# Performance work log

Hardware: AMD Instinct MI355X
Metric: run time of the kernel (lower is better)

Reference implementation:

```python
import jax, jax.numpy as jnp
import numpy as np
import math

D_MODEL = 1024
NUM_HEAD = 16
D_HEAD = D_MODEL // NUM_HEAD
SEQ = 2048
BATCH = 2


def setup_inputs() -> dict:
    key = jax.random.key(0)
    k1, k2, k3, k4, k5 = jax.random.split(key, 5)
    s = 1.0 / math.sqrt(D_MODEL)
    return {
        "x": jax.random.normal(k1, (SEQ, BATCH, D_MODEL), dtype=jnp.float32),
        "qkv_w": jax.random.normal(k2, (3 * D_MODEL, D_MODEL), dtype=jnp.float32) * s,
        "qkv_b": jax.random.normal(k3, (3 * D_MODEL,), dtype=jnp.float32) * 0.01,
        "out_w": jax.random.normal(k4, (D_MODEL, D_MODEL), dtype=jnp.float32) * s,
        "out_b": jax.random.normal(k5, (D_MODEL,), dtype=jnp.float32) * 0.01,
        "is_causal": 1,
    }


def reference(x, qkv_w, qkv_b, out_w, out_b, is_causal):
    t, b, _ = x.shape
    qkv = x @ qkv_w.T + qkv_b  # [t, b, 3*d_model]
    # 't b (k h d) -> b k h t d'
    qkv = qkv.reshape(t, b, 3, NUM_HEAD, D_HEAD).transpose(1, 2, 3, 0, 4)
    q, k, v = qkv[:, 0], qkv[:, 1], qkv[:, 2]  # each [b, h, t, d]
    softmax_scale = 1.0 / math.sqrt(D_HEAD)
    # NOTE: faithful to source bug: score is DIVIDED by softmax_scale
    score = jnp.einsum('bhtd,bhsd->bhts', q, k) / softmax_scale
    if is_causal:
        causal_mask = jnp.triu(jnp.full((t, t), -1000000.0, dtype=score.dtype), k=1)
        score = score + causal_mask
    attn = jax.nn.softmax(score, axis=-1)
    av = jnp.einsum('bhts,bhsd->bhtd', attn, v)  # [b, h, t, d]
    av = av.transpose(2, 0, 1, 3).reshape(t, b, D_MODEL)  # 'b h t d -> t b (h d)'
    return av @ out_w.T + out_b
```

## Files before the change

kernel.cpp:

```cpp
#include <hip/hip_runtime.h>
#include <math.h>

#define TSEQ   2048
#define BB     2
#define DMODEL 1024
#define NHEAD  16
#define DHEAD  64
#define MROWS  (TSEQ * BB)
#define NQB    (TSEQ / 64)

typedef __attribute__((ext_vector_type(8))) _Float16 half8;
typedef __attribute__((ext_vector_type(4))) float    floatx4;
typedef unsigned short u16;
typedef unsigned int   u32;

#define QSCL 11.5415603f
#define MSK  1442695.0f

__device__ __forceinline__ u16 f2h(float f) {
    union { _Float16 h; u16 u; } cv;
    cv.h = (_Float16)f;
    return cv.u;
}

__device__ __forceinline__ u32 pkrtz(float a, float b) {
    typedef __attribute__((ext_vector_type(2))) __fp16 fp16x2;
    union { fp16x2 h; u32 u; } cv;
    cv.h = __builtin_amdgcn_cvt_pkrtz(a, b);
    return cv.u;
}

__device__ __forceinline__ void async_cp16(const u16* g, u16* l) {
    __builtin_amdgcn_global_load_lds(
        (const __attribute__((address_space(1))) unsigned int*)g,
        (__attribute__((address_space(3))) unsigned int*)l, 16, 0, 0);
}

__global__ __launch_bounds__(256)
void cast3_f32_f16(const float* __restrict__ a, u16* __restrict__ oa,
                   const float* __restrict__ b, u16* __restrict__ ob,
                   const float* __restrict__ c, u16* __restrict__ oc)
{
    int i = blockIdx.x * 256 + threadIdx.x;
    const float* src; u16* dst; int off;
    if (i < 1048576)      { src = a; dst = oa; off = 0; }
    else if (i < 1835008) { src = b; dst = ob; off = 1048576; }
    else                  { src = c; dst = oc; off = 1835008; }
    int j = i - off;
    float4 v = ((const float4*)src)[j];
    ushort4 o;
    o.x = f2h(v.x); o.y = f2h(v.y); o.z = f2h(v.z); o.w = f2h(v.w);
    ((ushort4*)dst)[j] = o;
}

__global__ __launch_bounds__(256)
void gemm_qkv(const u16* __restrict__ A, const u16* __restrict__ W,
              const float* __restrict__ bias,
              u16* __restrict__ Qo, u16* __restrict__ Ko, u16* __restrict__ Vo,
              int M, int N, int K)
{
    __shared__ __align__(16) u16 As[128][64];
    __shared__ __align__(16) u16 Bs[64][64];

    const int tid  = threadIdx.x;
    const int lane = tid & 63;
    const int wv   = tid >> 6;
    const int ln   = lane & 15, lh = lane >> 4;
    const int m0   = blockIdx.y * 128;
    const int n0   = blockIdx.x * 64;

    const int c = n0 >> 10;
    const bool vmode = (c == 2);

    const int srowA = wv * 32 + (lane >> 3);
    const int srowW = wv * 16 + (lane >> 3);
    const int sslot = lane & 7;

    const floatx4 zero4 = {0.0f, 0.0f, 0.0f, 0.0f};
    floatx4 acc[2][4];
#pragma unroll
    for (int i = 0; i < 2; ++i)
#pragma unroll
        for (int j = 0; j < 4; ++j) acc[i][j] = zero4;

    for (int k0 = 0; k0 < K; k0 += 64) {
        __syncthreads();
#pragma unroll
        for (int t = 0; t < 4; ++t) {
            const int row = srowA + t * 8;
            const int g   = sslot ^ (row & 7);
            async_cp16(A + (size_t)(m0 + row) * K + k0 + g * 8, &As[row][sslot * 8]);
        }
#pragma unroll
        for (int t = 0; t < 2; ++t) {
            const int row = srowW + t * 8;
            const int g   = sslot ^ (row & 7);
            async_cp16(W + (size_t)(n0 + row) * K + k0 + g * 8, &Bs[row][sslot * 8]);
        }
        __syncthreads();

#pragma unroll
        for (int ks = 0; ks < 2; ++ks) {
            half8 xf[2], wf[4];
#pragma unroll
            for (int i = 0; i < 2; ++i) {
                const int row = wv * 32 + i * 16 + ln;
                xf[i] = *(const half8*)&As[row][(((ks << 2) | lh) ^ (row & 7)) * 8];
            }
#pragma unroll
            for (int j = 0; j < 4; ++j) {
                const int row = j * 16 + ln;
                wf[j] = *(const half8*)&Bs[row][(((ks << 2) | lh) ^ (row & 7)) * 8];
            }
            if (vmode) {
#pragma unroll
                for (int i = 0; i < 2; ++i)
#pragma unroll
                    for (int j = 0; j < 4; ++j)
                        acc[i][j] = __builtin_amdgcn_mfma_f32_16x16x32_f16(xf[i], wf[j], acc[i][j], 0, 0, 0);
            } else {
#pragma unroll
                for (int i = 0; i < 2; ++i)
#pragma unroll
                    for (int j = 0; j < 4; ++j)
                        acc[i][j] = __builtin_amdgcn_mfma_f32_16x16x32_f16(wf[j], xf[i], acc[i][j], 0, 0, 0);
            }
        }
    }

    if (!vmode) {
        const float scl = (c == 0) ? QSCL : 1.0f;
        u16* dst = (c == 0) ? Qo : Ko;
#pragma unroll
        for (int j = 0; j < 4; ++j) {
            const int nb = n0 + j * 16 + lh * 4;
            const float4 b4 = *(const float4*)&bias[nb];
            const int h  = (nb >> 6) & 15;
            const int d0 = nb & 63;
#pragma unroll
            for (int i = 0; i < 2; ++i) {
                const int tok = m0 + wv * 32 + i * 16 + ln;
                const int t = tok >> 1, b = tok & 1;
                uint2 pk;
                pk.x = pkrtz((acc[i][j][0] + b4.x) * scl, (acc[i][j][1] + b4.y) * scl);
                pk.y = pkrtz((acc[i][j][2] + b4.z) * scl, (acc[i][j][3] + b4.w) * scl);
                *(uint2*)&dst[(((size_t)b * NHEAD + h) * TSEQ + t) * DHEAD + d0] = pk;
            }
        }
    } else {
#pragma unroll
        for (int j = 0; j < 4; ++j) {
            const int col = n0 + j * 16 + ln;
            const float bc = bias[col];
            const int h = (col >> 6) & 15;
            const int d = col & 63;
#pragma unroll
            for (int i = 0; i < 2; ++i) {
                const int mb = m0 + wv * 32 + i * 16 + lh * 4;
                const int t0 = mb >> 1;
                const u32 e0 = pkrtz(acc[i][j][0] + bc, acc[i][j][2] + bc);
                const u32 e1 = pkrtz(acc[i][j][1] + bc, acc[i][j][3] + bc);
                *(u32*)&Vo[(((size_t)0 * NHEAD + h) * DHEAD + d) * TSEQ + t0] = e0;
                *(u32*)&Vo[(((size_t)1 * NHEAD + h) * DHEAD + d) * TSEQ + t0] = e1;
            }
        }
    }
}

__global__ __launch_bounds__(256)
void gemm_out64(const u16* __restrict__ A, const u16* __restrict__ W,
                const float* __restrict__ bias, float* __restrict__ Cout,
                int M, int N, int K)
{
    __shared__ __align__(16) u16 As[64][64];
    __shared__ __align__(16) u16 Bs[64][64];

    const int tid  = threadIdx.x;
    const int lane = tid & 63;
    const int wv   = tid >> 6;
    const int ln   = lane & 15, lh = lane >> 4;
    const int m0   = blockIdx.y * 64;
    const int n0   = blockIdx.x * 64;

    const floatx4 zero4 = {0.0f, 0.0f, 0.0f, 0.0f};
    floatx4 acc[4];
#pragma unroll
    for (int j = 0; j < 4; ++j) acc[j] = zero4;

    for (int k0 = 0; k0 < K; k0 += 64) {
        __syncthreads();
#pragma unroll
        for (int cb = 0; cb < 2; ++cb) {
            const int idx  = cb * 256 + tid;
            const int row  = idx >> 3;
            const int slot = idx & 7;
            const int g    = slot ^ (row & 7);
            async_cp16(A + (size_t)(m0 + row) * K + k0 + g * 8, &As[row][slot * 8]);
            async_cp16(W + (size_t)(n0 + row) * K + k0 + g * 8, &Bs[row][slot * 8]);
        }
        __syncthreads();

#pragma unroll
        for (int ks = 0; ks < 2; ++ks) {
            const int arow = wv * 16 + ln;
            half8 xf = *(const half8*)&As[arow][(((ks << 2) | lh) ^ (arow & 7)) * 8];
#pragma unroll
            for (int j = 0; j < 4; ++j) {
                const int row = j * 16 + ln;
                half8 wf = *(const half8*)&Bs[row][(((ks << 2) | lh) ^ (row & 7)) * 8];
                acc[j] = __builtin_amdgcn_mfma_f32_16x16x32_f16(wf, xf, acc[j], 0, 0, 0);
            }
        }
    }

#pragma unroll
    for (int j = 0; j < 4; ++j) {
        const int fb = n0 + j * 16 + lh * 4;
        const float4 b4 = *(const float4*)&bias[fb];
        const int tok = m0 + wv * 16 + ln;
        float4 v;
        v.x = acc[j][0] + b4.x;
        v.y = acc[j][1] + b4.y;
        v.z = acc[j][2] + b4.z;
        v.w = acc[j][3] + b4.w;
        *(float4*)&Cout[(size_t)tok * N + fb] = v;
    }
}

__global__ __launch_bounds__(256)
void flash_f16(const u16* __restrict__ Q, const u16* __restrict__ K,
               const u16* __restrict__ Vt, u16* __restrict__ AV,
               const int* __restrict__ causal_p)
{
    __shared__ __align__(16) u16 smem[(64 + 64 + 80) * 72];
    u16 (* __restrict__ QPs)[72] = (u16(*)[72])smem;
    u16 (* __restrict__ Ks)[72]  = (u16(*)[72])(smem + 64 * 72);
    u16 (* __restrict__ Vs)[72]  = (u16(*)[72])(smem + 128 * 72);

    const int tid  = threadIdx.x;
    const int lane = tid & 63;
    const int wv   = tid >> 6;
    const int ln   = lane & 15, lh = lane >> 4;

    const int phase = blockIdx.x >> 8;
    const int slot  = blockIdx.x & 255;
    const int bh    = slot & 31;
    const int jq    = slot >> 5;
    int qb;
    if      (phase == 0) qb = 31 - jq;
    else if (phase == 1) qb = jq;
    else if (phase == 2) qb = 23 - jq;
    else                 qb = 8 + jq;

    const int b = bh >> 4;
    const int h = bh & 15;
    const int causal = causal_p[0];

    const u16* Qg = Q  + (size_t)bh * TSEQ * DHEAD;
    const u16* Kg = K  + (size_t)bh * TSEQ * DHEAD;
    const u16* Vg = Vt + (size_t)bh * DHEAD * TSEQ;

    const int lrow = tid >> 3;
    const int lc8  = (tid & 7) * 8;

    *(uint4*)&QPs[lrow][lc8]      = *(const uint4*)(Qg + (size_t)(qb * 64 + lrow) * DHEAD + lc8);
    *(uint4*)&QPs[lrow + 32][lc8] = *(const uint4*)(Qg + (size_t)(qb * 64 + lrow + 32) * DHEAD + lc8);
    for (int idx = tid; idx < 16 * 72; idx += 256) {
        const int rr = idx / 72, cc = idx % 72;
        Vs[64 + rr][cc] = (rr == 0) ? (u16)0x3C00 : (u16)0;
    }
    uint4 kreg0 = *(const uint4*)(Kg + (size_t)lrow * DHEAD + lc8);
    uint4 kreg1 = *(const uint4*)(Kg + (size_t)(lrow + 32) * DHEAD + lc8);
    uint4 vreg0 = *(const uint4*)(Vg + (size_t)lrow * TSEQ + lc8);
    uint4 vreg1 = *(const uint4*)(Vg + (size_t)(lrow + 32) * TSEQ + lc8);
    __syncthreads();

    const int qr0  = wv * 16;
    const int qloc = qr0 + ln;
    const half8 bQ0 = *(const half8*)&QPs[qloc][lh * 8];
    const half8 bQ1 = *(const half8*)&QPs[qloc][32 + lh * 8];
    const half8 bO0 = *(const half8*)&Vs[64 + ln][lh * 8];
    const half8 bO1 = *(const half8*)&Vs[64 + ln][32 + lh * 8];

    const floatx4 zero4 = {0.0f, 0.0f, 0.0f, 0.0f};
    floatx4 o[4], o4;
#pragma unroll
    for (int j = 0; j < 4; ++j) o[j] = zero4;
    o4 = zero4;
    float m_i = -3.0e38f;

    const int kb_end = causal ? qb : (TSEQ / 64 - 1);
    for (int kb = 0; kb <= kb_end; ++kb) {
        *(uint4*)&Ks[lrow][lc8]      = kreg0;
        *(uint4*)&Ks[lrow + 32][lc8] = kreg1;
        *(uint4*)&Vs[lrow][lc8]      = vreg0;
        *(uint4*)&Vs[lrow + 32][lc8] = vreg1;
        __syncthreads();

        if (kb < kb_end) {
            const size_t nk = (size_t)(kb + 1) * 64;
            kreg0 = *(const uint4*)(Kg + (nk + lrow) * DHEAD + lc8);
            kreg1 = *(const uint4*)(Kg + (nk + lrow + 32) * DHEAD + lc8);
            vreg0 = *(const uint4*)(Vg + (size_t)lrow * TSEQ + nk + lc8);
            vreg1 = *(const uint4*)(Vg + (size_t)(lrow + 32) * TSEQ + nk + lc8);
        }

        floatx4 s[4];
#pragma unroll
        for (int j = 0; j < 4; ++j) {
            half8 aK0 = *(const half8*)&Ks[j * 16 + ln][lh * 8];
            half8 aK1 = *(const half8*)&Ks[j * 16 + ln][32 + lh * 8];
            floatx4 z = zero4;
            z = __builtin_amdgcn_mfma_f32_16x16x32_f16(aK0, bQ0, z, 0, 0, 0);
            z = __builtin_amdgcn_mfma_f32_16x16x32_f16(aK1, bQ1, z, 0, 0, 0);
            s[j] = z;
        }
        if ((causal != 0) && (kb == qb)) {
#pragma unroll
            for (int j = 0; j < 4; ++j)
#pragma unroll
                for (int r = 0; r < 4; ++r)
                    if (j * 16 + lh * 4 + r > qloc) s[j][r] -= MSK;
        }

        float mx = m_i;
#pragma unroll
        for (int j = 0; j < 4; ++j)
#pragma unroll
            for (int r = 0; r < 4; ++r) mx = fmaxf(mx, s[j][r]);
        mx = fmaxf(mx, __shfl_xor(mx, 16));
        mx = fmaxf(mx, __shfl_xor(mx, 32));
        const float alpha = exp2f(m_i - mx);
        m_i = mx;

#pragma unroll
        for (int j = 0; j < 4; ++j) {
            uint2 pk;
            pk.x = pkrtz(exp2f(s[j][0] - mx), exp2f(s[j][1] - mx));
            pk.y = pkrtz(exp2f(s[j][2] - mx), exp2f(s[j][3] - mx));
            *(uint2*)&QPs[qloc][j * 16 + lh * 4] = pk;
        }

        float a_r[4];
#pragma unroll
        for (int r = 0; r < 4; ++r) a_r[r] = __shfl(alpha, lh * 4 + r);
#pragma unroll
        for (int j = 0; j < 4; ++j)
#pragma unroll
            for (int r = 0; r < 4; ++r) o[j][r] *= a_r[r];
#pragma unroll
        for (int r = 0; r < 4; ++r) o4[r] *= a_r[r];

        half8 aP0 = *(const half8*)&QPs[qloc][lh * 8];
        half8 aP1 = *(const half8*)&QPs[qloc][32 + lh * 8];
#pragma unroll
        for (int j = 0; j < 4; ++j) {
            half8 bV0 = *(const half8*)&Vs[j * 16 + ln][lh * 8];
            half8 bV1 = *(const half8*)&Vs[j * 16 + ln][32 + lh * 8];
            o[j] = __builtin_amdgcn_mfma_f32_16x16x32_f16(aP0, bV0, o[j], 0, 0, 0);
            o[j] = __builtin_amdgcn_mfma_f32_16x16x32_f16(aP1, bV1, o[j], 0, 0, 0);
        }
        o4 = __builtin_amdgcn_mfma_f32_16x16x32_f16(aP0, bO0, o4, 0, 0, 0);
        o4 = __builtin_amdgcn_mfma_f32_16x16x32_f16(aP1, bO1, o4, 0, 0, 0);

        __syncthreads();
    }

#pragma unroll
    for (int r = 0; r < 4; ++r) {
        const float lr = __shfl(o4[r], lane & 48);
        const float il = 1.0f / lr;
        const int qrow = qb * 64 + qr0 + lh * 4 + r;
#pragma unroll
        for (int j = 0; j < 4; ++j) {
            const int d = j * 16 + ln;
            AV[((size_t)qrow * BB + b) * DMODEL + h * 64 + d] = f2h(o[j][r] * il);
        }
    }
}

extern "C" void kernel_launch(void* const* d_in, const int* in_sizes, int n_in,
                              void* d_out, int out_size, void* d_ws, size_t ws_size,
                              hipStream_t stream)
{
    const float* x      = (const float*)d_in[0];
    const float* qkv_w  = (const float*)d_in[1];
    const float* qkv_b  = (const float*)d_in[2];
    const float* out_w  = (const float*)d_in[3];
    const float* out_b  = (const float*)d_in[4];
    const int*   is_causal = (const int*)d_in[5];
    float* out = (float*)d_out;

    u16* ws   = (u16*)d_ws;
    u16* xb   = ws;
    u16* wqkv = xb   + (size_t)4194304;
    u16* wout = wqkv + (size_t)3145728;
    u16* Qh   = wout + (size_t)1048576;
    u16* Kh   = Qh   + (size_t)4194304;
    u16* Vth  = Kh   + (size_t)4194304;
    u16* AVh  = Vth  + (size_t)4194304;

    cast3_f32_f16<<<8192, 256, 0, stream>>>(x, xb, qkv_w, wqkv, out_w, wout);

    gemm_qkv<<<dim3(3 * DMODEL / 64, MROWS / 128), 256, 0, stream>>>(
        xb, wqkv, qkv_b, Qh, Kh, Vth, MROWS, 3 * DMODEL, DMODEL);

    flash_f16<<<1024, 256, 0, stream>>>(Qh, Kh, Vth, AVh, is_causal);

    gemm_out64<<<dim3(DMODEL / 64, MROWS / 64), 256, 0, stream>>>(
        AVh, wout, out_b, out, MROWS, DMODEL, DMODEL);
}
```

Measured before the change: 190.0 us.

## Prefetch next GEMM K-tile into registers to overlap loads with MFMA

Both the QKV projection GEMM and the output GEMM drop the synchronous global_load_lds copies. They now load the next K-tile into registers while MFMAs run on the current LDS tile, then write those registers to LDS after a barrier. This hides global-memory latency behind compute within each block, at the cost of extra VGPRs and explicit LDS stores. The XOR swizzle is kept and its source column is precomputed once per thread.

```diff
diff --git a/kernel.cpp b/kernel.cpp
--- a/kernel.cpp
+++ b/kernel.cpp
@@ -28,12 +28,6 @@
     union { fp16x2 h; u32 u; } cv;
     cv.h = __builtin_amdgcn_cvt_pkrtz(a, b);
     return cv.u;
-}
-
-__device__ __forceinline__ void async_cp16(const u16* g, u16* l) {
-    __builtin_amdgcn_global_load_lds(
-        (const __attribute__((address_space(1))) unsigned int*)g,
-        (__attribute__((address_space(3))) unsigned int*)l, 16, 0, 0);
 }
 
 __global__ __launch_bounds__(256)
@@ -75,6 +69,10 @@
     const int srowA = wv * 32 + (lane >> 3);
     const int srowW = wv * 16 + (lane >> 3);
     const int sslot = lane & 7;
+    const int gcol  = (sslot ^ ((lane >> 3) & 7)) * 8;
+
+    const u16* gA = A + (size_t)(m0 + srowA) * K + gcol;
+    const u16* gW = W + (size_t)(n0 + srowW) * K + gcol;
 
     const floatx4 zero4 = {0.0f, 0.0f, 0.0f, 0.0f};
     floatx4 acc[2][4];
@@ -83,21 +81,27 @@
 #pragma unroll
         for (int j = 0; j < 4; ++j) acc[i][j] = zero4;
 
-    for (int k0 = 0; k0 < K; k0 += 64) {
-        __syncthreads();
-#pragma unroll
-        for (int t = 0; t < 4; ++t) {
-            const int row = srowA + t * 8;
-            const int g   = sslot ^ (row & 7);
-            async_cp16(A + (size_t)(m0 + row) * K + k0 + g * 8, &As[row][sslot * 8]);
-        }
-#pragma unroll
-        for (int t = 0; t < 2; ++t) {
-            const int row = srowW + t * 8;
-            const int g   = sslot ^ (row & 7);
-            async_cp16(W + (size_t)(n0 + row) * K + k0 + g * 8, &Bs[row][sslot * 8]);
-        }
-        __syncthreads();
+    uint4 ra[4], rb[2];
+#pragma unroll
+    for (int t = 0; t < 4; ++t) ra[t] = *(const uint4*)(gA + (size_t)t * 8 * K);
+#pragma unroll
+    for (int t = 0; t < 2; ++t) rb[t] = *(const uint4*)(gW + (size_t)t * 8 * K);
+#pragma unroll
+    for (int t = 0; t < 4; ++t) *(uint4*)&As[srowA + t * 8][sslot * 8] = ra[t];
+#pragma unroll
+    for (int t = 0; t < 2; ++t) *(uint4*)&Bs[srowW + t * 8][sslot * 8] = rb[t];
+
+    const int NIT = K / 64;
+    for (int it = 0; it < NIT; ++it) {
+        __syncthreads();
+
+        if (it + 1 < NIT) {
+            const int k0 = (it + 1) * 64;
+#pragma unroll
+            for (int t = 0; t < 4; ++t) ra[t] = *(const uint4*)(gA + (size_t)t * 8 * K + k0);
+#pragma unroll
+            for (int t = 0; t < 2; ++t) rb[t] = *(const uint4*)(gW + (size_t)t * 8 * K + k0);
+        }
 
 #pragma unroll
         for (int ks = 0; ks < 2; ++ks) {
@@ -125,6 +129,14 @@
                     for (int j = 0; j < 4; ++j)
                         acc[i][j] = __builtin_amdgcn_mfma_f32_16x16x32_f16(wf[j], xf[i], acc[i][j], 0, 0, 0);
             }
+        }
+
+        __syncthreads();
+        if (it + 1 < NIT) {
+#pragma unroll
+            for (int t = 0; t < 4; ++t) *(uint4*)&As[srowA + t * 8][sslot * 8] = ra[t];
+#pragma unroll
+            for (int t = 0; t < 2; ++t) *(uint4*)&Bs[srowW + t * 8][sslot * 8] = rb[t];
         }
     }
 
@@ -182,23 +194,38 @@
     const int m0   = blockIdx.y * 64;
     const int n0   = blockIdx.x * 64;
 
+    const int srow  = tid >> 3;
+    const int sslot = tid & 7;
+    const int g0 = (sslot ^ (srow & 7)) * 8;
+    const int g1 = (sslot ^ ((srow + 32) & 7)) * 8;
+
+    const u16* gA0 = A + (size_t)(m0 + srow) * K + g0;
+    const u16* gA1 = A + (size_t)(m0 + srow + 32) * K + g1;
+    const u16* gW0 = W + (size_t)(n0 + srow) * K + g0;
+    const u16* gW1 = W + (size_t)(n0 + srow + 32) * K + g1;
+
     const floatx4 zero4 = {0.0f, 0.0f, 0.0f, 0.0f};
     floatx4 acc[4];
 #pragma unroll
     for (int j = 0; j < 4; ++j) acc[j] = zero4;
 
-    for (int k0 = 0; k0 < K; k0 += 64) {
-        __syncthreads();
-#pragma unroll
-        for (int cb = 0; cb < 2; ++cb) {
-            const int idx  = cb * 256 + tid;
-            const int row  = idx >> 3;
-            const int slot = idx & 7;
-            const int g    = slot ^ (row & 7);
-            async_cp16(A + (size_t)(m0 + row) * K + k0 + g * 8, &As[row][slot * 8]);
-            async_cp16(W + (size_t)(n0 + row) * K + k0 + g * 8, &Bs[row][slot * 8]);
-        }
-        __syncthreads();
+    uint4 ra0, ra1, rb0, rb1;
+    ra0 = *(const uint4*)gA0; ra1 = *(const uint4*)gA1;
+    rb0 = *(const uint4*)gW0; rb1 = *(const uint4*)gW1;
+    *(uint4*)&As[srow][sslot * 8]      = ra0;
+    *(uint4*)&As[srow + 32][sslot * 8] = ra1;
+    *(uint4*)&Bs[srow][sslot * 8]      = rb0;
+    *(uint4*)&Bs[srow + 32][sslot * 8] = rb1;
+
+    const int NIT = K / 64;
+    for (int it = 0; it < NIT; ++it) {
+        __syncthreads();
+
+        if (it + 1 < NIT) {
+            const int k0 = (it + 1) * 64;
+            ra0 = *(const uint4*)(gA0 + k0); ra1 = *(const uint4*)(gA1 + k0);
+            rb0 = *(const uint4*)(gW0 + k0); rb1 = *(const uint4*)(gW1 + k0);
+        }
 
 #pragma unroll
         for (int ks = 0; ks < 2; ++ks) {
@@ -210,6 +237,14 @@
                 half8 wf = *(const half8*)&Bs[row][(((ks << 2) | lh) ^ (row & 7)) * 8];
                 acc[j] = __builtin_amdgcn_mfma_f32_16x16x32_f16(wf, xf, acc[j], 0, 0, 0);
             }
+        }
+
+        __syncthreads();
+        if (it + 1 < NIT) {
+            *(uint4*)&As[srow][sslot * 8]      = ra0;
+            *(uint4*)&As[srow + 32][sslot * 8] = ra1;
+            *(uint4*)&Bs[srow][sslot * 8]      = rb0;
+            *(uint4*)&Bs[srow + 32][sslot * 8] = rb1;
         }
     }
 
```

After: 309.0 us. 62.7% more time.
